# Optimization experiments

Measured on AMD Instinct MI355X. Metric: run time of the kernel, lower is better.

The kernel has to match this reference:

```python
import jax, jax.numpy as jnp
import numpy as np

D = 1024
H = 16
HD = D // H
FF = 4 * D
EPS = 1e-5


def _layernorm(x, scale, shift):
    # Faithful to the torch module: unbiased std (ddof=1), eps added to std.
    mean = jnp.mean(x, axis=-1, keepdims=True)
    var = jnp.sum((x - mean) ** 2, axis=-1, keepdims=True) / (x.shape[-1] - 1)
    std = jnp.sqrt(var)
    return shift + scale * (x - mean) / (std + EPS)


def _gelu(x):
    c = jnp.sqrt(jnp.asarray(2.0 / jnp.pi, dtype=x.dtype))
    return 0.5 * x * (1.0 + jnp.tanh(c * (x + 0.044715 * x ** 3)))


def setup_inputs() -> dict:
    key = jax.random.key(0)
    ks = jax.random.split(key, 8)
    B, S = 2, 2048
    inv = 1.0 / np.sqrt(D)
    x = jax.random.normal(ks[0], (B, S, D), dtype=jnp.float32)
    scale1 = jnp.ones((D,), jnp.float32)
    shift1 = jnp.zeros((D,), jnp.float32)
    Wqkv = jax.random.normal(ks[1], (3 * D, D), jnp.float32) * inv  # torch layout [out,in]
    Wo_w = jax.random.normal(ks[2], (D, D), jnp.float32) * inv
    Wo_b = jnp.zeros((D,), jnp.float32)
    scale2 = jnp.ones((D,), jnp.float32)
    shift2 = jnp.zeros((D,), jnp.float32)
    W1 = jax.random.normal(ks[3], (FF, D), jnp.float32) * inv
    b1 = jnp.zeros((FF,), jnp.float32)
    W2 = jax.random.normal(ks[4], (D, FF), jnp.float32) * (1.0 / np.sqrt(FF))
    b2 = jnp.zeros((D,), jnp.float32)
    return {"x": x, "scale1": scale1, "shift1": shift1, "Wqkv": Wqkv,
            "Wo_w": Wo_w, "Wo_b": Wo_b, "scale2": scale2, "shift2": shift2,
            "W1": W1, "b1": b1, "W2": W2, "b2": b2}


def reference(x, scale1, shift1, Wqkv, Wo_w, Wo_b, scale2, shift2, W1, b1, W2, b2):
    B, S, _ = x.shape
    # --- pre-norm attention ---
    h = _layernorm(x, scale1, shift1)
    qkv = jnp.einsum('bsd,ed->bse', h, Wqkv)  # [B,S,3D]
    q, k, v = jnp.split(qkv, 3, axis=-1)
    q = q.reshape(B, S, H, HD).transpose(0, 2, 1, 3)  # [B,H,S,HD]
    k = k.reshape(B, S, H, HD).transpose(0, 2, 1, 3)
    v = v.reshape(B, S, H, HD).transpose(0, 2, 1, 3)
    scores = jnp.einsum('bhqd,bhkd->bhqk', q, k) / jnp.sqrt(jnp.asarray(HD, x.dtype))
    causal = jnp.triu(jnp.ones((S, S), dtype=bool), k=1)
    scores = jnp.where(causal, -jnp.inf, scores)
    weights = jax.nn.softmax(scores, axis=-1)
    attn = jnp.einsum('bhqk,bhkd->bhqd', weights, v)
    attn = attn.transpose(0, 2, 1, 3).reshape(B, S, D)
    attn = jnp.einsum('bsd,ed->bse', attn, Wo_w) + Wo_b
    x = x + attn
    # --- pre-norm MLP ---
    h2 = _layernorm(x, scale2, shift2)
    m = _gelu(jnp.einsum('bsd,fd->bsf', h2, W1) + b1)
    m = jnp.einsum('bsf,df->bsd', m, W2) + b2
    return x + m
```

## Files before the change

kernel.cpp:

```cpp
#include <hip/hip_runtime.h>
#include <cstdint>
#include <cstddef>

typedef __bf16 bf16;
typedef __bf16 v8bf __attribute__((ext_vector_type(8)));
typedef __bf16 v4bf __attribute__((ext_vector_type(4)));
typedef float  v4f  __attribute__((ext_vector_type(4)));

#define D_MODEL 1024
#define FF_DIM  4096
#define SEQ     2048
#define NTOK    4096
#define NH      16
#define HDIM    64

#define GLOAD_LDS16(g, l) \
    __builtin_amdgcn_global_load_lds((const __attribute__((address_space(1))) void*)(g), \
                                     (__attribute__((address_space(3))) void*)(l), 16, 0, 0)

#define QSCALE 0.18033688011112042f
#define SHIFT2 -28.853900817779268f

#define BARRIER()    asm volatile("s_barrier" ::: "memory")
#define WAIT_VM8()   asm volatile("s_waitcnt vmcnt(8)" ::: "memory")
#define WAIT_VM0()   asm volatile("s_waitcnt vmcnt(0)" ::: "memory")
#define WAIT_LGKM0() asm volatile("s_waitcnt lgkmcnt(0)" ::: "memory")

__global__ __launch_bounds__(256) void prep_kernel(
    const float* __restrict__ Wqkv, const float* __restrict__ Wo,
    const float* __restrict__ W1, const float* __restrict__ W2,
    bf16* __restrict__ Wqkv_b, bf16* __restrict__ Wo_b,
    bf16* __restrict__ W1_b, bf16* __restrict__ W2_b) {
    int u = blockIdx.x * 256 + threadIdx.x;
    const float* src; bf16* dst; int idx;
    if (u < 786432)       { src = Wqkv; dst = Wqkv_b; idx = u * 4; }
    else if (u < 1048576) { src = Wo;   dst = Wo_b;   idx = (u - 786432) * 4; }
    else if (u < 2097152) { src = W1;   dst = W1_b;   idx = (u - 1048576) * 4; }
    else                  { src = W2;   dst = W2_b;   idx = (u - 2097152) * 4; }
    float4 v = *(const float4*)(src + idx);
    dst[idx + 0] = (bf16)v.x;
    dst[idx + 1] = (bf16)v.y;
    dst[idx + 2] = (bf16)v.z;
    dst[idx + 3] = (bf16)v.w;
}

__global__ __launch_bounds__(256) void layernorm_kernel(
    const float* __restrict__ x, const float* __restrict__ scale,
    const float* __restrict__ shift, bf16* __restrict__ out) {
    int row = blockIdx.x;
    int t = threadIdx.x;
    const float* xr = x + (size_t)row * D_MODEL;
    float4 v = *(const float4*)(xr + t * 4);
    float s  = v.x + v.y + v.z + v.w;
    float sq = v.x * v.x + v.y * v.y + v.z * v.z + v.w * v.w;
    #pragma unroll
    for (int o = 1; o < 64; o <<= 1) {
        s  += __shfl_xor(s, o);
        sq += __shfl_xor(sq, o);
    }
    __shared__ float ws[8];
    int wv = t >> 6;
    if ((t & 63) == 0) { ws[wv * 2] = s; ws[wv * 2 + 1] = sq; }
    __syncthreads();
    s  = ws[0] + ws[2] + ws[4] + ws[6];
    sq = ws[1] + ws[3] + ws[5] + ws[7];
    float mean = s * (1.0f / D_MODEL);
    float var  = (sq - (float)D_MODEL * mean * mean) * (1.0f / (D_MODEL - 1));
    var = fmaxf(var, 0.0f);
    float inv = 1.0f / (sqrtf(var) + 1e-5f);
    #pragma unroll
    for (int j = 0; j < 4; ++j) {
        int c = t * 4 + j;
        float xv = (&v.x)[j];
        out[(size_t)row * D_MODEL + c] = (bf16)(shift[c] + scale[c] * (xv - mean) * inv);
    }
}

__global__ __launch_bounds__(256) void transpose_v(
    const bf16* __restrict__ vb, bf16* __restrict__ vt) {
    int bh = blockIdx.x >> 5;
    int ts = blockIdx.x & 31;
    int t = threadIdx.x;
    __shared__ bf16 T[64][72];
    const bf16* src = vb + ((size_t)bh * SEQ + ts * 64) * HDIM;
    #pragma unroll
    for (int half = 0; half < 2; ++half) {
        int s = (t >> 3) + half * 32;
        int d0 = (t & 7) * 8;
        v8bf vv = *(const v8bf*)(src + (size_t)s * HDIM + d0);
        #pragma unroll
        for (int j = 0; j < 8; ++j) T[d0 + j][s] = vv[j];
    }
    __syncthreads();
    bf16* dst = vt + (size_t)bh * HDIM * SEQ + ts * 64;
    int d = t >> 2;
    #pragma unroll
    for (int cc = 0; cc < 2; ++cc) {
        int c = (t & 3) + cc * 4;
        v8bf o = *(const v8bf*)(&T[d][c * 8]);
        *(v8bf*)(dst + (size_t)d * SEQ + c * 8) = o;
    }
}

template <int EPI>
__global__ __launch_bounds__(256) void gemm_nt(
    const bf16* __restrict__ A, const bf16* __restrict__ Bw,
    const float* __restrict__ bias, const float* __restrict__ resid,
    float* __restrict__ outf, bf16* __restrict__ ob0,
    bf16* __restrict__ ob1, bf16* __restrict__ ob2,
    int M, int N, int K, int klen) {
    __shared__ __align__(16) bf16 As[128 * 64];
    __shared__ __align__(16) bf16 Bs[128 * 64];
    int gx = gridDim.x;
    int lin = blockIdx.y * gx + blockIdx.x;
    int grpsz = 16 * gx;
    int group = lin / grpsz;
    int rem = lin - group * grpsz;
    int m_t = group * 16 + (rem & 15);
    int n_t = rem >> 4;
    int m0 = m_t * 128, n0 = n_t * 128;
    int kstart = blockIdx.z * klen;
    int t = threadIdx.x;
    int lane = t & 63, wave = t >> 6;
    int wm = wave >> 1, wn = wave & 1;
    int quad = lane >> 4, l16 = lane & 15;

    int srow8 = lane >> 3;
    int schunk = (lane & 7) ^ srow8;
    const bf16* agp = A  + (size_t)(m0 + wave * 8 + srow8) * K + kstart + schunk * 8;
    const bf16* bgp = Bw + (size_t)(n0 + wave * 8 + srow8) * K + kstart + schunk * 8;
    size_t row32 = (size_t)32 * K;

    v4f acc[4][4];
    #pragma unroll
    for (int i = 0; i < 4; ++i)
        #pragma unroll
        for (int j = 0; j < 4; ++j)
            acc[i][j] = (v4f){0.f, 0.f, 0.f, 0.f};

    int rsw = l16 & 7;
    for (int kk = 0; kk < klen; kk += 64) {
        __syncthreads();
        #pragma unroll
        for (int ii = 0; ii < 4; ++ii) {
            GLOAD_LDS16(agp + ii * row32 + kk, &As[ii * 2048 + wave * 512]);
            GLOAD_LDS16(bgp + ii * row32 + kk, &Bs[ii * 2048 + wave * 512]);
        }
        __syncthreads();
        #pragma unroll
        for (int h = 0; h < 2; ++h) {
            v8bf af[4], bfr[4];
            #pragma unroll
            for (int i = 0; i < 4; ++i)
                af[i] = *(const v8bf*)(&As[(wm * 64 + i * 16 + l16) * 64 + (((h * 4 + quad) ^ rsw)) * 8]);
            #pragma unroll
            for (int j = 0; j < 4; ++j)
                bfr[j] = *(const v8bf*)(&Bs[(wn * 64 + j * 16 + l16) * 64 + (((h * 4 + quad) ^ rsw)) * 8]);
            #pragma unroll
            for (int i = 0; i < 4; ++i)
                #pragma unroll
                for (int j = 0; j < 4; ++j)
                    acc[i][j] = __builtin_amdgcn_mfma_f32_16x16x32_bf16(af[i], bfr[j], acc[i][j], 0, 0, 0);
        }
    }

    #pragma unroll
    for (int i = 0; i < 4; ++i) {
        #pragma unroll
        for (int j = 0; j < 4; ++j) {
            #pragma unroll
            for (int r = 0; r < 4; ++r) {
                float v = acc[i][j][r];
                int row = m0 + wm * 64 + i * 16 + quad * 4 + r;
                int col = n0 + wn * 64 + j * 16 + l16;
                if (EPI == 1) {
                    size_t o = (size_t)row * N + col;
                    outf[o] = resid[o] + v + bias[col];
                }
            }
        }
    }
}

template <int EPI>
__global__ __launch_bounds__(512, 2) void gemm2_nt(
    const bf16* __restrict__ A, const bf16* __restrict__ Bw,
    const float* __restrict__ bias, bf16* __restrict__ ob0,
    bf16* __restrict__ ob1, bf16* __restrict__ ob2,
    int M, int N, int K, int klen) {
    __shared__ __align__(16) bf16 smA[2][256 * 64];
    __shared__ __align__(16) bf16 smB[2][256 * 64];

    int m0 = blockIdx.y * 256, n0 = blockIdx.x * 256;
    int kstart = blockIdx.z * klen;
    int t = threadIdx.x;
    int lane = t & 63, wave = t >> 6;
    int wm = wave >> 2, wn = wave & 3;
    int quad = lane >> 4, l16 = lane & 15;

    int srow8 = lane >> 3;
    int schunk = (lane & 7) ^ srow8;
    const bf16* aA = A  + (size_t)(m0 + wave * 8 + srow8) * K + kstart + schunk * 8;
    const bf16* bB = Bw + (size_t)(n0 + wave * 8 + srow8) * K + kstart + schunk * 8;
    size_t row64 = (size_t)64 * K;
    int NT = klen >> 6;

    v4f acc[8][4];
    #pragma unroll
    for (int i = 0; i < 8; ++i)
        #pragma unroll
        for (int j = 0; j < 4; ++j)
            acc[i][j] = (v4f){0.f, 0.f, 0.f, 0.f};

    auto stage = [&](int c, int kt) {
        size_t ko = (size_t)kt * 64;
        const bf16* ag = aA + ko;
        const bf16* bg = bB + ko;
        #pragma unroll
        for (int q = 0; q < 4; ++q) {
            GLOAD_LDS16(ag + q * row64, &smA[c][q * 4096 + wave * 512]);
            GLOAD_LDS16(bg + q * row64, &smB[c][q * 4096 + wave * 512]);
        }
    };

    stage(0, 0);
    if (NT > 1) { stage(1, 1); WAIT_VM8(); } else { WAIT_VM0(); }
    BARRIER();

    int rx = l16 & 7;
    int ch0 = (quad ^ rx) * 8;
    int ch1 = ch0 ^ 32;
    int arow = (wm * 128 + l16) * 64;
    int brow = (wn * 64 + l16) * 64;

    for (int kt = 0; kt < NT; ++kt) {
        int c = kt & 1;
        const bf16* Ab = &smA[c][arow];
        const bf16* Bb = &smB[c][brow];
        v8bf a[4][2], b[4][2];
        #pragma unroll
        for (int i = 0; i < 4; ++i) {
            a[i][0] = *(const v8bf*)(Ab + i * 1024 + ch0);
            a[i][1] = *(const v8bf*)(Ab + i * 1024 + ch1);
        }
        #pragma unroll
        for (int j = 0; j < 4; ++j) {
            b[j][0] = *(const v8bf*)(Bb + j * 1024 + ch0);
            b[j][1] = *(const v8bf*)(Bb + j * 1024 + ch1);
        }
        __builtin_amdgcn_s_setprio(1);
        #pragma unroll
        for (int i = 0; i < 4; ++i)
            #pragma unroll
            for (int j = 0; j < 2; ++j) {
                acc[i][j] = __builtin_amdgcn_mfma_f32_16x16x32_bf16(a[i][0], b[j][0], acc[i][j], 0, 0, 0);
                acc[i][j] = __builtin_amdgcn_mfma_f32_16x16x32_bf16(a[i][1], b[j][1], acc[i][j], 0, 0, 0);
            }
        __builtin_amdgcn_s_setprio(0);
        __builtin_amdgcn_s_setprio(1);
        #pragma unroll
        for (int i = 0; i < 4; ++i)
            #pragma unroll
            for (int j = 2; j < 4; ++j) {
                acc[i][j] = __builtin_amdgcn_mfma_f32_16x16x32_bf16(a[i][0], b[j][0], acc[i][j], 0, 0, 0);
                acc[i][j] = __builtin_amdgcn_mfma_f32_16x16x32_bf16(a[i][1], b[j][1], acc[i][j], 0, 0, 0);
            }
        __builtin_amdgcn_s_setprio(0);
        #pragma unroll
        for (int i = 0; i < 4; ++i) {
            a[i][0] = *(const v8bf*)(Ab + 4096 + i * 1024 + ch0);
            a[i][1] = *(const v8bf*)(Ab + 4096 + i * 1024 + ch1);
        }
        __builtin_amdgcn_s_setprio(1);
        #pragma unroll
        for (int i = 0; i < 4; ++i)
            #pragma unroll
            for (int j = 0; j < 2; ++j) {
                acc[i + 4][j] = __builtin_amdgcn_mfma_f32_16x16x32_bf16(a[i][0], b[j][0], acc[i + 4][j], 0, 0, 0);
                acc[i + 4][j] = __builtin_amdgcn_mfma_f32_16x16x32_bf16(a[i][1], b[j][1], acc[i + 4][j], 0, 0, 0);
            }
        __builtin_amdgcn_s_setprio(0);
        WAIT_LGKM0();
        BARRIER();
        if (kt + 2 < NT) stage(c, kt + 2);
        __builtin_amdgcn_s_setprio(1);
        #pragma unroll
        for (int i = 0; i < 4; ++i)
            #pragma unroll
            for (int j = 2; j < 4; ++j) {
                acc[i + 4][j] = __builtin_amdgcn_mfma_f32_16x16x32_bf16(a[i][0], b[j][0], acc[i + 4][j], 0, 0, 0);
                acc[i + 4][j] = __builtin_amdgcn_mfma_f32_16x16x32_bf16(a[i][1], b[j][1], acc[i + 4][j], 0, 0, 0);
            }
        __builtin_amdgcn_s_setprio(0);
        if (kt + 1 < NT) {
            if (kt + 2 < NT) WAIT_VM8();
            else             WAIT_VM0();
            BARRIER();
        }
    }

    #pragma unroll
    for (int i = 0; i < 8; ++i) {
        #pragma unroll
        for (int j = 0; j < 4; ++j) {
            #pragma unroll
            for (int r = 0; r < 4; ++r) {
                float v = acc[i][j][r];
                int row = m0 + wm * 128 + i * 16 + quad * 4 + r;
                int col = n0 + wn * 64 + j * 16 + l16;
                if (EPI == 0) {
                    int which = col >> 10, rr = col & 1023;
                    int h = rr >> 6, d = rr & 63;
                    int bb = row >> 11, sI = row & 2047;
                    size_t dst = (((size_t)(bb * NH + h)) * SEQ + sI) * HDIM + d;
                    if (which == 0)      ob0[dst] = (bf16)(v * QSCALE);
                    else if (which == 1) ob1[dst] = (bf16)v;
                    else                 ob2[dst] = (bf16)v;
                } else if (EPI == 2) {
                    float u = v + bias[col];
                    float y = 1.5957691216057308f * (u + 0.044715f * u * u * u);
                    float g = u * __builtin_amdgcn_rcpf(1.0f + __expf(-y));
                    ob0[(size_t)row * N + col] = (bf16)g;
                } else {
                    ob0[(size_t)blockIdx.z * M * N + (size_t)row * N + col] = (bf16)v;
                }
            }
        }
    }
}

__global__ __launch_bounds__(256) void combine_w2(
    const bf16* __restrict__ part, const float* __restrict__ x1,
    const float* __restrict__ b2, float* __restrict__ out) {
    int i = (blockIdx.x * 256 + threadIdx.x) * 4;
    int col = i & (D_MODEL - 1);
    float4 xv = *(const float4*)(x1 + i);
    float4 bv = *(const float4*)(b2 + col);
    float4 r;
    r.x = xv.x + bv.x; r.y = xv.y + bv.y; r.z = xv.z + bv.z; r.w = xv.w + bv.w;
    #pragma unroll
    for (int z = 0; z < 4; ++z) {
        v4bf p = *(const v4bf*)(part + (size_t)z * NTOK * D_MODEL + i);
        r.x += (float)p[0]; r.y += (float)p[1]; r.z += (float)p[2]; r.w += (float)p[3];
    }
    *(float4*)(out + i) = r;
}

__device__ __forceinline__ void attn_process_tile(
    int kv, int qwb, int quad, int l16,
    const bf16* Ks, const bf16* Vs, bf16* Pw,
    const v8bf& qf0, const v8bf& qf1, v4f (&o)[4], float& lsum) {
    #pragma unroll
    for (int hh = 0; hh < 2; ++hh) {
        int kb32 = kv + hh * 32;
        if (kb32 > qwb + 15) break;
        #pragma unroll
        for (int j2 = 0; j2 < 2; ++j2) {
            int j = hh * 2 + j2;
            int kb16 = kb32 + j2 * 16;
            union { bf16 h[4]; uint2 u; } pk;
            if (kb16 > qwb + 15) {
                pk.u = (uint2){0u, 0u};
            } else {
                int key = j * 16 + l16;
                v8bf ka = *(const v8bf*)(&Ks[(key * 8 + (quad ^ (key & 7))) * 8]);
                v8bf kc = *(const v8bf*)(&Ks[(key * 8 + ((quad + 4) ^ (key & 7))) * 8]);
                v4f s = (v4f){SHIFT2, SHIFT2, SHIFT2, SHIFT2};
                s = __builtin_amdgcn_mfma_f32_16x16x32_bf16(ka, qf0, s, 0, 0, 0);
                s = __builtin_amdgcn_mfma_f32_16x16x32_bf16(kc, qf1, s, 0, 0, 0);
                bool dm = (kb16 + 15 > qwb);
                int keyb = kb16 + quad * 4;
                #pragma unroll
                for (int r = 0; r < 4; ++r) {
                    float pv = __builtin_amdgcn_exp2f(s[r]);
                    if (dm) pv = (keyb + r <= qwb + l16) ? pv : 0.f;
                    lsum += pv;
                    pk.h[r] = (bf16)pv;
                }
            }
            *(uint2*)(&Pw[l16 * 80 + j * 16 + quad * 4]) = pk.u;
        }
        v8bf pf = *(const v8bf*)(&Pw[l16 * 80 + hh * 32 + quad * 8]);
        #pragma unroll
        for (int dc = 0; dc < 4; ++dc) {
            int dim = dc * 16 + l16;
            v8bf vv = *(const v8bf*)(&Vs[(dim * 8 + ((quad + 4 * hh) ^ (dim & 7))) * 8]);
            o[dc] = __builtin_amdgcn_mfma_f32_16x16x32_bf16(pf, vv, o[dc], 0, 0, 0);
        }
    }
}

__global__ __launch_bounds__(256) void attn_kernel(
    const bf16* __restrict__ qb, const bf16* __restrict__ kb,
    const bf16* __restrict__ vt, bf16* __restrict__ ob) {
    int bh = blockIdx.x & 31;
    int pr = blockIdx.x >> 5;
    int qtA = pr, qtB = 31 - pr;

    int t = threadIdx.x;
    int wave = t >> 6, lane = t & 63;
    int quad = lane >> 4, l16 = lane & 15;
    int qwbA = qtA * 64 + wave * 16;
    int qwbB = qtB * 64 + wave * 16;

    const bf16* Qh  = qb + (size_t)bh * SEQ * HDIM;
    const bf16* Kh  = kb + (size_t)bh * SEQ * HDIM;
    const bf16* Vth = vt + (size_t)bh * HDIM * SEQ;

    __shared__ __align__(16) bf16 Ks[64 * 64];
    __shared__ __align__(16) bf16 Vs[64 * 64];
    __shared__ __align__(16) bf16 Ps[4][16 * 80];
    bf16* Pw = &Ps[wave][0];

    int u0 = t, u1 = t + 256;
    int key0 = u0 >> 3, c0 = (u0 & 7) ^ (key0 & 7);
    int key1 = u1 >> 3, c1 = (u1 & 7) ^ (key1 & 7);
    bf16* kdst0 = &Ks[wave * 512];
    bf16* kdst1 = &Ks[2048 + wave * 512];
    bf16* vdst0 = &Vs[wave * 512];
    bf16* vdst1 = &Vs[2048 + wave * 512];
    const bf16* Ksrc0 = Kh + (size_t)key0 * HDIM + c0 * 8;
    const bf16* Ksrc1 = Kh + (size_t)key1 * HDIM + c1 * 8;
    const bf16* Vsrc0 = Vth + (size_t)key0 * SEQ + c0 * 8;
    const bf16* Vsrc1 = Vth + (size_t)key1 * SEQ + c1 * 8;

    v8bf qfA0 = *(const v8bf*)(Qh + (size_t)(qwbA + l16) * HDIM + quad * 8);
    v8bf qfA1 = *(const v8bf*)(Qh + (size_t)(qwbA + l16) * HDIM + 32 + quad * 8);
    v8bf qfB0 = *(const v8bf*)(Qh + (size_t)(qwbB + l16) * HDIM + quad * 8);
    v8bf qfB1 = *(const v8bf*)(Qh + (size_t)(qwbB + l16) * HDIM + 32 + quad * 8);

    v4f oA[4], oB[4];
    #pragma unroll
    for (int dc = 0; dc < 4; ++dc) {
        oA[dc] = (v4f){0.f, 0.f, 0.f, 0.f};
        oB[dc] = (v4f){0.f, 0.f, 0.f, 0.f};
    }
    float lA = 0.f, lB = 0.f;

    int kvendA = qtA * 64 + 64;
    int kvendB = qtB * 64 + 64;
    for (int kv = 0; kv < kvendB; kv += 64) {
        __syncthreads();
        GLOAD_LDS16(Ksrc0 + (size_t)kv * HDIM, kdst0);
        GLOAD_LDS16(Ksrc1 + (size_t)kv * HDIM, kdst1);
        GLOAD_LDS16(Vsrc0 + kv, vdst0);
        GLOAD_LDS16(Vsrc1 + kv, vdst1);
        __syncthreads();
        if (kv < kvendA)
            attn_process_tile(kv, qwbA, quad, l16, Ks, Vs, Pw, qfA0, qfA1, oA, lA);
        attn_process_tile(kv, qwbB, quad, l16, Ks, Vs, Pw, qfB0, qfB1, oB, lB);
    }

    lA += __shfl_xor(lA, 16); lA += __shfl_xor(lA, 32);
    lB += __shfl_xor(lB, 16); lB += __shfl_xor(lB, 32);

    int b = bh >> 4, h = bh & 15;
    #pragma unroll
    for (int r = 0; r < 4; ++r) {
        float invA = 1.0f / __shfl(lA, quad * 4 + r);
        float invB = 1.0f / __shfl(lB, quad * 4 + r);
        int sA = qwbA + quad * 4 + r;
        int sB = qwbB + quad * 4 + r;
        #pragma unroll
        for (int dc = 0; dc < 4; ++dc) {
            int d = dc * 16 + l16;
            ob[((size_t)(b * SEQ + sA)) * D_MODEL + h * HDIM + d] = (bf16)(oA[dc][r] * invA);
            ob[((size_t)(b * SEQ + sB)) * D_MODEL + h * HDIM + d] = (bf16)(oB[dc][r] * invB);
        }
    }
}

extern "C" void kernel_launch(void* const* d_in, const int* in_sizes, int n_in,
                              void* d_out, int out_size, void* d_ws, size_t ws_size,
                              hipStream_t stream) {
    const float* x      = (const float*)d_in[0];
    const float* scale1 = (const float*)d_in[1];
    const float* shift1 = (const float*)d_in[2];
    const float* Wqkv   = (const float*)d_in[3];
    const float* Wo_w   = (const float*)d_in[4];
    const float* Wo_b   = (const float*)d_in[5];
    const float* scale2 = (const float*)d_in[6];
    const float* shift2 = (const float*)d_in[7];
    const float* W1     = (const float*)d_in[8];
    const float* b1     = (const float*)d_in[9];
    const float* W2     = (const float*)d_in[10];
    const float* b2     = (const float*)d_in[11];
    float* out = (float*)d_out;

    char* ws = (char*)d_ws;
    size_t off = 0;
    auto alloc = [&](size_t bytes) -> char* {
        char* p = ws + off;
        off += (bytes + 255) & ~(size_t)255;
        return p;
    };
    bf16* Wqkv_b = (bf16*)alloc((size_t)3 * D_MODEL * D_MODEL * 2);
    bf16* Wo_bf  = (bf16*)alloc((size_t)D_MODEL * D_MODEL * 2);
    bf16* W1_b   = (bf16*)alloc((size_t)FF_DIM * D_MODEL * 2);
    bf16* W2_b   = (bf16*)alloc((size_t)D_MODEL * FF_DIM * 2);
    bf16* bufA   = (bf16*)alloc((size_t)NTOK * D_MODEL * 2);
    bf16* qb     = (bf16*)alloc((size_t)NTOK * D_MODEL * 2);
    bf16* kb     = (bf16*)alloc((size_t)NTOK * D_MODEL * 2);
    bf16* vb     = (bf16*)alloc((size_t)NTOK * D_MODEL * 2);
    bf16* vtb    = (bf16*)alloc((size_t)NTOK * D_MODEL * 2);
    float* x1    = (float*)alloc((size_t)NTOK * D_MODEL * 4);
    bf16* mbuf   = (bf16*)alloc((size_t)NTOK * FF_DIM * 2);
    bf16* w2part = bufA;
    (void)ws_size; (void)n_in; (void)in_sizes; (void)out_size;

    prep_kernel<<<12288, 256, 0, stream>>>(Wqkv, Wo_w, W1, W2,
                                           Wqkv_b, Wo_bf, W1_b, W2_b);

    layernorm_kernel<<<NTOK, 256, 0, stream>>>(x, scale1, shift1, bufA);

    gemm2_nt<0><<<dim3(3072 / 256, NTOK / 256), 512, 0, stream>>>(
        bufA, Wqkv_b, nullptr, qb, kb, vb, NTOK, 3072, D_MODEL, D_MODEL);

    transpose_v<<<1024, 256, 0, stream>>>(vb, vtb);

    attn_kernel<<<512, 256, 0, stream>>>(qb, kb, vtb, bufA);

    gemm_nt<1><<<dim3(D_MODEL / 128, NTOK / 128), 256, 0, stream>>>(
        bufA, Wo_bf, Wo_b, x, x1, nullptr, nullptr, nullptr, NTOK, D_MODEL, D_MODEL, D_MODEL);

    layernorm_kernel<<<NTOK, 256, 0, stream>>>(x1, scale2, shift2, qb);

    gemm2_nt<2><<<dim3(FF_DIM / 256, NTOK / 256), 512, 0, stream>>>(
        qb, W1_b, b1, mbuf, nullptr, nullptr, NTOK, FF_DIM, D_MODEL, D_MODEL);

    gemm2_nt<6><<<dim3(D_MODEL / 256, NTOK / 256, 4), 512, 0, stream>>>(
        mbuf, W2_b, nullptr, w2part, nullptr, nullptr, NTOK, D_MODEL, FF_DIM, FF_DIM / 4);

    combine_w2<<<NTOK * D_MODEL / 1024, 256, 0, stream>>>(w2part, x1, b2, out);
}
```

Baseline: 323.8 us.

## Double-buffer attention K/V tiles and fuse paired query-tile processing

The attention kernel now keeps two LDS buffers for K/V tiles and prefetches the tile two steps ahead with global-to-LDS loads, using vmcnt waits so the next tile's load overlaps the current tile's compute. The two query tiles (A and B) are processed together per key-tile, sharing the K and V fragment reads from LDS and interleaving their MFMAs. The P scratch buffers are split per query tile and XOR-swizzled to reduce LDS bank conflicts. In exchange it doubles LDS use and adds register pressure, which may lower occupancy.

```diff
diff --git a/kernel.cpp b/kernel.cpp
--- a/kernel.cpp
+++ b/kernel.cpp
@@ -23,6 +23,7 @@
 
 #define BARRIER()    asm volatile("s_barrier" ::: "memory")
 #define WAIT_VM8()   asm volatile("s_waitcnt vmcnt(8)" ::: "memory")
+#define WAIT_VM4()   asm volatile("s_waitcnt vmcnt(4)" ::: "memory")
 #define WAIT_VM0()   asm volatile("s_waitcnt vmcnt(0)" ::: "memory")
 #define WAIT_LGKM0() asm volatile("s_waitcnt lgkmcnt(0)" ::: "memory")
 
@@ -346,46 +347,82 @@
     *(float4*)(out + i) = r;
 }
 
-__device__ __forceinline__ void attn_process_tile(
-    int kv, int qwb, int quad, int l16,
-    const bf16* Ks, const bf16* Vs, bf16* Pw,
-    const v8bf& qf0, const v8bf& qf1, v4f (&o)[4], float& lsum) {
+__device__ __forceinline__ void attn_tile_pair(
+    int kv, int qwbA, int qwbB, bool doA, int quad, int l16, int sw,
+    const bf16* Ks, const bf16* Vs, bf16* PwA, bf16* PwB,
+    const v8bf& qfA0, const v8bf& qfA1, const v8bf& qfB0, const v8bf& qfB1,
+    v4f (&oA)[4], v4f (&oB)[4], float& lA, float& lB) {
     #pragma unroll
     for (int hh = 0; hh < 2; ++hh) {
         int kb32 = kv + hh * 32;
-        if (kb32 > qwb + 15) break;
+        if (kb32 > qwbB + 15) break;
+        bool aH = doA && (kb32 <= qwbA + 15);
         #pragma unroll
         for (int j2 = 0; j2 < 2; ++j2) {
             int j = hh * 2 + j2;
             int kb16 = kb32 + j2 * 16;
-            union { bf16 h[4]; uint2 u; } pk;
-            if (kb16 > qwb + 15) {
-                pk.u = (uint2){0u, 0u};
-            } else {
-                int key = j * 16 + l16;
-                v8bf ka = *(const v8bf*)(&Ks[(key * 8 + (quad ^ (key & 7))) * 8]);
-                v8bf kc = *(const v8bf*)(&Ks[(key * 8 + ((quad + 4) ^ (key & 7))) * 8]);
-                v4f s = (v4f){SHIFT2, SHIFT2, SHIFT2, SHIFT2};
-                s = __builtin_amdgcn_mfma_f32_16x16x32_bf16(ka, qf0, s, 0, 0, 0);
-                s = __builtin_amdgcn_mfma_f32_16x16x32_bf16(kc, qf1, s, 0, 0, 0);
-                bool dm = (kb16 + 15 > qwb);
-                int keyb = kb16 + quad * 4;
-                #pragma unroll
-                for (int r = 0; r < 4; ++r) {
-                    float pv = __builtin_amdgcn_exp2f(s[r]);
-                    if (dm) pv = (keyb + r <= qwb + l16) ? pv : 0.f;
-                    lsum += pv;
-                    pk.h[r] = (bf16)pv;
+            int key = j * 16 + l16;
+            v8bf ka = *(const v8bf*)(&Ks[(key * 8 + (quad ^ (key & 7))) * 8]);
+            v8bf kc = *(const v8bf*)(&Ks[(key * 8 + ((quad + 4) ^ (key & 7))) * 8]);
+            int poff = l16 * 80 + ((j * 4 + quad) ^ sw) * 4;
+            int keyb = kb16 + quad * 4;
+            {
+                union { bf16 h[4]; uint2 u; } pk;
+                if (kb16 > qwbB + 15) {
+                    pk.u = (uint2){0u, 0u};
+                } else {
+                    v4f s = (v4f){SHIFT2, SHIFT2, SHIFT2, SHIFT2};
+                    s = __builtin_amdgcn_mfma_f32_16x16x32_bf16(ka, qfB0, s, 0, 0, 0);
+                    s = __builtin_amdgcn_mfma_f32_16x16x32_bf16(kc, qfB1, s, 0, 0, 0);
+                    bool dm = (kb16 + 15 > qwbB);
+                    #pragma unroll
+                    for (int r = 0; r < 4; ++r) {
+                        float pv = __builtin_amdgcn_exp2f(s[r]);
+                        if (dm) pv = (keyb + r <= qwbB + l16) ? pv : 0.f;
+                        lB += pv;
+                        pk.h[r] = (bf16)pv;
+                    }
                 }
-            }
-            *(uint2*)(&Pw[l16 * 80 + j * 16 + quad * 4]) = pk.u;
-        }
-        v8bf pf = *(const v8bf*)(&Pw[l16 * 80 + hh * 32 + quad * 8]);
-        #pragma unroll
-        for (int dc = 0; dc < 4; ++dc) {
-            int dim = dc * 16 + l16;
-            v8bf vv = *(const v8bf*)(&Vs[(dim * 8 + ((quad + 4 * hh) ^ (dim & 7))) * 8]);
-            o[dc] = __builtin_amdgcn_mfma_f32_16x16x32_bf16(pf, vv, o[dc], 0, 0, 0);
+                *(uint2*)(&PwB[poff]) = pk.u;
+            }
+            if (aH) {
+                union { bf16 h[4]; uint2 u; } pk;
+                if (kb16 > qwbA + 15) {
+                    pk.u = (uint2){0u, 0u};
+                } else {
+                    v4f s = (v4f){SHIFT2, SHIFT2, SHIFT2, SHIFT2};
+                    s = __builtin_amdgcn_mfma_f32_16x16x32_bf16(ka, qfA0, s, 0, 0, 0);
+                    s = __builtin_amdgcn_mfma_f32_16x16x32_bf16(kc, qfA1, s, 0, 0, 0);
+                    bool dm = (kb16 + 15 > qwbA);
+                    #pragma unroll
+                    for (int r = 0; r < 4; ++r) {
+                        float pv = __builtin_amdgcn_exp2f(s[r]);
+                        if (dm) pv = (keyb + r <= qwbA + l16) ? pv : 0.f;
+                        lA += pv;
+                        pk.h[r] = (bf16)pv;
+                    }
+                }
+                *(uint2*)(&PwA[poff]) = pk.u;
+            }
+        }
+        int roff = l16 * 80 + (((hh * 4 + quad) * 2) ^ sw) * 4;
+        v8bf pfB = *(const v8bf*)(&PwB[roff]);
+        if (aH) {
+            v8bf pfA = *(const v8bf*)(&PwA[roff]);
+            #pragma unroll
+            for (int dc = 0; dc < 4; ++dc) {
+                int dim = dc * 16 + l16;
+                v8bf vv = *(const v8bf*)(&Vs[(dim * 8 + ((quad + 4 * hh) ^ (dim & 7))) * 8]);
+                oB[dc] = __builtin_amdgcn_mfma_f32_16x16x32_bf16(pfB, vv, oB[dc], 0, 0, 0);
+                oA[dc] = __builtin_amdgcn_mfma_f32_16x16x32_bf16(pfA, vv, oA[dc], 0, 0, 0);
+            }
+        } else {
+            #pragma unroll
+            for (int dc = 0; dc < 4; ++dc) {
+                int dim = dc * 16 + l16;
+                v8bf vv = *(const v8bf*)(&Vs[(dim * 8 + ((quad + 4 * hh) ^ (dim & 7))) * 8]);
+                oB[dc] = __builtin_amdgcn_mfma_f32_16x16x32_bf16(pfB, vv, oB[dc], 0, 0, 0);
+            }
         }
     }
 }
@@ -400,6 +437,7 @@
     int t = threadIdx.x;
     int wave = t >> 6, lane = t & 63;
     int quad = lane >> 4, l16 = lane & 15;
+    int sw = l16 & 12;
     int qwbA = qtA * 64 + wave * 16;
     int qwbB = qtB * 64 + wave * 16;
 
@@ -407,23 +445,27 @@
     const bf16* Kh  = kb + (size_t)bh * SEQ * HDIM;
     const bf16* Vth = vt + (size_t)bh * HDIM * SEQ;
 
-    __shared__ __align__(16) bf16 Ks[64 * 64];
-    __shared__ __align__(16) bf16 Vs[64 * 64];
-    __shared__ __align__(16) bf16 Ps[4][16 * 80];
-    bf16* Pw = &Ps[wave][0];
+    __shared__ __align__(16) bf16 Ks[2][64 * 64];
+    __shared__ __align__(16) bf16 Vs[2][64 * 64];
+    __shared__ __align__(16) bf16 Ps[4][2][16 * 80];
+    bf16* PwA = &Ps[wave][0][0];
+    bf16* PwB = &Ps[wave][1][0];
 
     int u0 = t, u1 = t + 256;
     int key0 = u0 >> 3, c0 = (u0 & 7) ^ (key0 & 7);
     int key1 = u1 >> 3, c1 = (u1 & 7) ^ (key1 & 7);
-    bf16* kdst0 = &Ks[wave * 512];
-    bf16* kdst1 = &Ks[2048 + wave * 512];
-    bf16* vdst0 = &Vs[wave * 512];
-    bf16* vdst1 = &Vs[2048 + wave * 512];
     const bf16* Ksrc0 = Kh + (size_t)key0 * HDIM + c0 * 8;
     const bf16* Ksrc1 = Kh + (size_t)key1 * HDIM + c1 * 8;
     const bf16* Vsrc0 = Vth + (size_t)key0 * SEQ + c0 * 8;
     const bf16* Vsrc1 = Vth + (size_t)key1 * SEQ + c1 * 8;
 
+    auto stage = [&](int c, int kv) {
+        GLOAD_LDS16(Ksrc0 + (size_t)kv * HDIM, &Ks[c][wave * 512]);
+        GLOAD_LDS16(Ksrc1 + (size_t)kv * HDIM, &Ks[c][2048 + wave * 512]);
+        GLOAD_LDS16(Vsrc0 + kv, &Vs[c][wave * 512]);
+        GLOAD_LDS16(Vsrc1 + kv, &Vs[c][2048 + wave * 512]);
+    };
+
     v8bf qfA0 = *(const v8bf*)(Qh + (size_t)(qwbA + l16) * HDIM + quad * 8);
     v8bf qfA1 = *(const v8bf*)(Qh + (size_t)(qwbA + l16) * HDIM + 32 + quad * 8);
     v8bf qfB0 = *(const v8bf*)(Qh + (size_t)(qwbB + l16) * HDIM + quad * 8);
@@ -437,18 +479,27 @@
     }
     float lA = 0.f, lB = 0.f;
 
-    int kvendA = qtA * 64 + 64;
-    int kvendB = qtB * 64 + 64;
-    for (int kv = 0; kv < kvendB; kv += 64) {
-        __syncthreads();
-        GLOAD_LDS16(Ksrc0 + (size_t)kv * HDIM, kdst0);
-        GLOAD_LDS16(Ksrc1 + (size_t)kv * HDIM, kdst1);
-        GLOAD_LDS16(Vsrc0 + kv, vdst0);
-        GLOAD_LDS16(Vsrc1 + kv, vdst1);
-        __syncthreads();
-        if (kv < kvendA)
-            attn_process_tile(kv, qwbA, quad, l16, Ks, Vs, Pw, qfA0, qfA1, oA, lA);
-        attn_process_tile(kv, qwbB, quad, l16, Ks, Vs, Pw, qfB0, qfB1, oB, lB);
+    int nt = qtB + 1;
+    stage(0, 0);
+    stage(1, 64);
+    WAIT_VM4();
+    BARRIER();
+
+    for (int ti = 0; ti < nt; ++ti) {
+        int c = ti & 1;
+        int kv = ti * 64;
+        bool doA = (ti <= qtA);
+        attn_tile_pair(kv, qwbA, qwbB, doA, quad, l16, sw,
+                       &Ks[c][0], &Vs[c][0], PwA, PwB,
+                       qfA0, qfA1, qfB0, qfB1, oA, oB, lA, lB);
+        WAIT_LGKM0();
+        BARRIER();
+        if (ti + 2 < nt) stage(c, kv + 128);
+        if (ti + 1 < nt) {
+            if (ti + 2 < nt) WAIT_VM4();
+            else             WAIT_VM0();
+            BARRIER();
+        }
     }
 
     lA += __shfl_xor(lA, 16); lA += __shfl_xor(lA, 32);
```

Result: slower. 331.2 us (+2.3%).

## Split attention KV tiles across two wave groups and compute row sums via MFMA

Applied to the files above, without the earlier changes.

The attention kernel now runs 512 threads as two groups of four waves. Each group handles alternate 64-key tiles, loaded together into a doubled K/V shared buffer, and the partial outputs are reduced through shared memory at the end. The per-element softmax row-sum accumulation is replaced by an extra MFMA of P against a ones vector, which removes scalar adds and cross-lane shuffles. This raises parallelism per block and trades more LDS use and a final reduction for fewer serial KV iterations.

```diff
diff --git a/kernel.cpp b/kernel.cpp
--- a/kernel.cpp
+++ b/kernel.cpp
@@ -348,8 +348,8 @@
 
 __device__ __forceinline__ void attn_process_tile(
     int kv, int qwb, int quad, int l16,
-    const bf16* Ks, const bf16* Vs, bf16* Pw,
-    const v8bf& qf0, const v8bf& qf1, v4f (&o)[4], float& lsum) {
+    const bf16* Ks, const bf16* Vs, bf16* Pw, const v8bf& ones,
+    const v8bf& qf0, const v8bf& qf1, v4f (&o)[4], v4f& o5) {
     #pragma unroll
     for (int hh = 0; hh < 2; ++hh) {
         int kb32 = kv + hh * 32;
@@ -374,13 +374,13 @@
                 for (int r = 0; r < 4; ++r) {
                     float pv = __builtin_amdgcn_exp2f(s[r]);
                     if (dm) pv = (keyb + r <= qwb + l16) ? pv : 0.f;
-                    lsum += pv;
                     pk.h[r] = (bf16)pv;
                 }
             }
             *(uint2*)(&Pw[l16 * 80 + j * 16 + quad * 4]) = pk.u;
         }
         v8bf pf = *(const v8bf*)(&Pw[l16 * 80 + hh * 32 + quad * 8]);
+        o5 = __builtin_amdgcn_mfma_f32_16x16x32_bf16(pf, ones, o5, 0, 0, 0);
         #pragma unroll
         for (int dc = 0; dc < 4; ++dc) {
             int dim = dc * 16 + l16;
@@ -390,7 +390,7 @@
     }
 }
 
-__global__ __launch_bounds__(256) void attn_kernel(
+__global__ __launch_bounds__(512, 4) void attn_kernel(
     const bf16* __restrict__ qb, const bf16* __restrict__ kb,
     const bf16* __restrict__ vt, bf16* __restrict__ ob) {
     int bh = blockIdx.x & 31;
@@ -399,73 +399,117 @@
 
     int t = threadIdx.x;
     int wave = t >> 6, lane = t & 63;
+    int g = wave >> 2, wv = wave & 3;
     int quad = lane >> 4, l16 = lane & 15;
-    int qwbA = qtA * 64 + wave * 16;
-    int qwbB = qtB * 64 + wave * 16;
+    int qwbA = qtA * 64 + wv * 16;
+    int qwbB = qtB * 64 + wv * 16;
 
     const bf16* Qh  = qb + (size_t)bh * SEQ * HDIM;
     const bf16* Kh  = kb + (size_t)bh * SEQ * HDIM;
     const bf16* Vth = vt + (size_t)bh * HDIM * SEQ;
 
-    __shared__ __align__(16) bf16 Ks[64 * 64];
-    __shared__ __align__(16) bf16 Vs[64 * 64];
-    __shared__ __align__(16) bf16 Ps[4][16 * 80];
-    bf16* Pw = &Ps[wave][0];
-
-    int u0 = t, u1 = t + 256;
-    int key0 = u0 >> 3, c0 = (u0 & 7) ^ (key0 & 7);
-    int key1 = u1 >> 3, c1 = (u1 & 7) ^ (key1 & 7);
-    bf16* kdst0 = &Ks[wave * 512];
-    bf16* kdst1 = &Ks[2048 + wave * 512];
-    bf16* vdst0 = &Vs[wave * 512];
-    bf16* vdst1 = &Vs[2048 + wave * 512];
-    const bf16* Ksrc0 = Kh + (size_t)key0 * HDIM + c0 * 8;
-    const bf16* Ksrc1 = Kh + (size_t)key1 * HDIM + c1 * 8;
-    const bf16* Vsrc0 = Vth + (size_t)key0 * SEQ + c0 * 8;
-    const bf16* Vsrc1 = Vth + (size_t)key1 * SEQ + c1 * 8;
+    __shared__ __align__(16) char smem_raw[53248];
+    bf16* Ks  = (bf16*)smem_raw;
+    bf16* Vs  = (bf16*)(smem_raw + 16384);
+    bf16* Pw  = (bf16*)(smem_raw + 32768) + wave * 1280;
+    float* scr = (float*)smem_raw;
+
+    int key = t >> 3;
+    int cch = (t & 7) ^ (key & 7);
+    const bf16* Ksrc = Kh + (size_t)key * HDIM + cch * 8;
+    const bf16* Vsrc = Vth + (size_t)key * SEQ + cch * 8;
+    bf16* kdst0 = Ks + wave * 512;
+    bf16* kdst1 = Ks + 4096 + wave * 512;
+    bf16* vdst0 = Vs + wave * 512;
+    bf16* vdst1 = Vs + 4096 + wave * 512;
 
     v8bf qfA0 = *(const v8bf*)(Qh + (size_t)(qwbA + l16) * HDIM + quad * 8);
     v8bf qfA1 = *(const v8bf*)(Qh + (size_t)(qwbA + l16) * HDIM + 32 + quad * 8);
     v8bf qfB0 = *(const v8bf*)(Qh + (size_t)(qwbB + l16) * HDIM + quad * 8);
     v8bf qfB1 = *(const v8bf*)(Qh + (size_t)(qwbB + l16) * HDIM + 32 + quad * 8);
 
+    v8bf ones;
+    #pragma unroll
+    for (int j = 0; j < 8; ++j) ones[j] = (bf16)1.0f;
+
     v4f oA[4], oB[4];
     #pragma unroll
     for (int dc = 0; dc < 4; ++dc) {
         oA[dc] = (v4f){0.f, 0.f, 0.f, 0.f};
         oB[dc] = (v4f){0.f, 0.f, 0.f, 0.f};
     }
-    float lA = 0.f, lB = 0.f;
-
-    int kvendA = qtA * 64 + 64;
-    int kvendB = qtB * 64 + 64;
-    for (int kv = 0; kv < kvendB; kv += 64) {
+    v4f o5A = (v4f){0.f, 0.f, 0.f, 0.f};
+    v4f o5B = (v4f){0.f, 0.f, 0.f, 0.f};
+
+    int nt = qtB + 1;
+    int nit = (nt + 1) >> 1;
+    for (int it = 0; it < nit; ++it) {
+        int t0 = 2 * it;
+        int t1 = t0 + 1;
         __syncthreads();
-        GLOAD_LDS16(Ksrc0 + (size_t)kv * HDIM, kdst0);
-        GLOAD_LDS16(Ksrc1 + (size_t)kv * HDIM, kdst1);
-        GLOAD_LDS16(Vsrc0 + kv, vdst0);
-        GLOAD_LDS16(Vsrc1 + kv, vdst1);
+        GLOAD_LDS16(Ksrc + (size_t)(t0 * 64) * HDIM, kdst0);
+        GLOAD_LDS16(Vsrc + t0 * 64, vdst0);
+        if (t1 < nt) {
+            GLOAD_LDS16(Ksrc + (size_t)(t1 * 64) * HDIM, kdst1);
+            GLOAD_LDS16(Vsrc + t1 * 64, vdst1);
+        }
         __syncthreads();
-        if (kv < kvendA)
-            attn_process_tile(kv, qwbA, quad, l16, Ks, Vs, Pw, qfA0, qfA1, oA, lA);
-        attn_process_tile(kv, qwbB, quad, l16, Ks, Vs, Pw, qfB0, qfB1, oB, lB);
-    }
-
-    lA += __shfl_xor(lA, 16); lA += __shfl_xor(lA, 32);
-    lB += __shfl_xor(lB, 16); lB += __shfl_xor(lB, 32);
-
-    int b = bh >> 4, h = bh & 15;
-    #pragma unroll
-    for (int r = 0; r < 4; ++r) {
-        float invA = 1.0f / __shfl(lA, quad * 4 + r);
-        float invB = 1.0f / __shfl(lB, quad * 4 + r);
-        int sA = qwbA + quad * 4 + r;
-        int sB = qwbB + quad * 4 + r;
-        #pragma unroll
-        for (int dc = 0; dc < 4; ++dc) {
-            int d = dc * 16 + l16;
-            ob[((size_t)(b * SEQ + sA)) * D_MODEL + h * HDIM + d] = (bf16)(oA[dc][r] * invA);
-            ob[((size_t)(b * SEQ + sB)) * D_MODEL + h * HDIM + d] = (bf16)(oB[dc][r] * invB);
+        int ti = t0 + g;
+        if (ti < nt) {
+            int kv = ti * 64;
+            const bf16* Kst = Ks + g * 4096;
+            const bf16* Vst = Vs + g * 4096;
+            if (ti <= qtA)
+                attn_process_tile(kv, qwbA, quad, l16, Kst, Vst, Pw, ones,
+                                  qfA0, qfA1, oA, o5A);
+            attn_process_tile(kv, qwbB, quad, l16, Kst, Vst, Pw, ones,
+                              qfB0, qfB1, oB, o5B);
+        }
+    }
+
+    __syncthreads();
+    int sbase = wv * 2560 + lane;
+    if (g == 1) {
+        #pragma unroll
+        for (int dc = 0; dc < 4; ++dc)
+            #pragma unroll
+            for (int r = 0; r < 4; ++r) {
+                scr[sbase + (dc * 4 + r) * 64]        = oA[dc][r];
+                scr[sbase + (16 + dc * 4 + r) * 64]   = oB[dc][r];
+            }
+        #pragma unroll
+        for (int r = 0; r < 4; ++r) {
+            scr[sbase + (32 + r) * 64] = o5A[r];
+            scr[sbase + (36 + r) * 64] = o5B[r];
+        }
+    }
+    __syncthreads();
+    if (g == 0) {
+        #pragma unroll
+        for (int dc = 0; dc < 4; ++dc)
+            #pragma unroll
+            for (int r = 0; r < 4; ++r) {
+                oA[dc][r] += scr[sbase + (dc * 4 + r) * 64];
+                oB[dc][r] += scr[sbase + (16 + dc * 4 + r) * 64];
+            }
+        #pragma unroll
+        for (int r = 0; r < 4; ++r) {
+            o5A[r] += scr[sbase + (32 + r) * 64];
+            o5B[r] += scr[sbase + (36 + r) * 64];
+        }
+        int b = bh >> 4, h = bh & 15;
+        #pragma unroll
+        for (int r = 0; r < 4; ++r) {
+            float invA = 1.0f / o5A[r];
+            float invB = 1.0f / o5B[r];
+            int sA = qwbA + quad * 4 + r;
+            int sB = qwbB + quad * 4 + r;
+            #pragma unroll
+            for (int dc = 0; dc < 4; ++dc) {
+                int d = dc * 16 + l16;
+                ob[((size_t)(b * SEQ + sA)) * D_MODEL + h * HDIM + d] = (bf16)(oA[dc][r] * invA);
+                ob[((size_t)(b * SEQ + sB)) * D_MODEL + h * HDIM + d] = (bf16)(oB[dc][r] * invB);
+            }
         }
     }
 }
@@ -518,7 +562,7 @@
 
     transpose_v<<<1024, 256, 0, stream>>>(vb, vtb);
 
-    attn_kernel<<<512, 256, 0, stream>>>(qb, kb, vtb, bufA);
+    attn_kernel<<<512, 512, 0, stream>>>(qb, kb, vtb, bufA);
 
     gemm_nt<1><<<dim3(D_MODEL / 128, NTOK / 128), 256, 0, stream>>>(
         bufA, Wo_bf, Wo_b, x, x1, nullptr, nullptr, nullptr, NTOK, D_MODEL, D_MODEL, D_MODEL);
```

Measured after the change: 313.4 us. -3.2%, faster.

## Double-buffer attention KV tiles, one q-tile per block, MFMA row sums, swizzle GEMM grid

Applied to the files above, without the earlier changes.

The attention kernel changes from pairing two query tiles per block to one query tile per block, launching 1024 blocks in heaviest-first order. K/V tiles are now double-buffered in LDS with global_load_lds prefetch and vmcnt waits, so loads overlap compute. The softmax denominator is computed with an MFMA against a ones vector instead of scalar adds and shuffles, and the P row stride shrinks to 72. The bf16 GEMM also remaps workgroup IDs with an XCD-style swizzle to improve L2 locality. The trade-offs are more LDS per block and a possible loss of load balance from the unpaired tiles.

```diff
diff --git a/kernel.cpp b/kernel.cpp
--- a/kernel.cpp
+++ b/kernel.cpp
@@ -23,6 +23,7 @@
 
 #define BARRIER()    asm volatile("s_barrier" ::: "memory")
 #define WAIT_VM8()   asm volatile("s_waitcnt vmcnt(8)" ::: "memory")
+#define WAIT_VM4()   asm volatile("s_waitcnt vmcnt(4)" ::: "memory")
 #define WAIT_VM0()   asm volatile("s_waitcnt vmcnt(0)" ::: "memory")
 #define WAIT_LGKM0() asm volatile("s_waitcnt lgkmcnt(0)" ::: "memory")
 
@@ -191,7 +192,14 @@
     __shared__ __align__(16) bf16 smA[2][256 * 64];
     __shared__ __align__(16) bf16 smB[2][256 * 64];
 
-    int m0 = blockIdx.y * 256, n0 = blockIdx.x * 256;
+    int gx = gridDim.x, gy = gridDim.y;
+    int nwg = gx * gy;
+    int lin = blockIdx.y * gx + blockIdx.x;
+    int q8 = nwg >> 3;
+    int swz = (lin & 7) * q8 + (lin >> 3);
+    int m_t = swz % gy;
+    int n_t = swz / gy;
+    int m0 = m_t * 256, n0 = n_t * 256;
     int kstart = blockIdx.z * klen;
     int t = threadIdx.x;
     int lane = t & 63, wave = t >> 6;
@@ -348,8 +356,8 @@
 
 __device__ __forceinline__ void attn_process_tile(
     int kv, int qwb, int quad, int l16,
-    const bf16* Ks, const bf16* Vs, bf16* Pw,
-    const v8bf& qf0, const v8bf& qf1, v4f (&o)[4], float& lsum) {
+    const bf16* Ks, const bf16* Vs, bf16* Pw, const v8bf& ones,
+    const v8bf& qf0, const v8bf& qf1, v4f (&o)[4], v4f& o5) {
     #pragma unroll
     for (int hh = 0; hh < 2; ++hh) {
         int kb32 = kv + hh * 32;
@@ -374,13 +382,13 @@
                 for (int r = 0; r < 4; ++r) {
                     float pv = __builtin_amdgcn_exp2f(s[r]);
                     if (dm) pv = (keyb + r <= qwb + l16) ? pv : 0.f;
-                    lsum += pv;
                     pk.h[r] = (bf16)pv;
                 }
             }
-            *(uint2*)(&Pw[l16 * 80 + j * 16 + quad * 4]) = pk.u;
-        }
-        v8bf pf = *(const v8bf*)(&Pw[l16 * 80 + hh * 32 + quad * 8]);
+            *(uint2*)(&Pw[l16 * 72 + j * 16 + quad * 4]) = pk.u;
+        }
+        v8bf pf = *(const v8bf*)(&Pw[l16 * 72 + hh * 32 + quad * 8]);
+        o5 = __builtin_amdgcn_mfma_f32_16x16x32_bf16(pf, ones, o5, 0, 0, 0);
         #pragma unroll
         for (int dc = 0; dc < 4; ++dc) {
             int dim = dc * 16 + l16;
@@ -390,82 +398,75 @@
     }
 }
 
-__global__ __launch_bounds__(256) void attn_kernel(
+__global__ __launch_bounds__(256, 4) void attn_kernel(
     const bf16* __restrict__ qb, const bf16* __restrict__ kb,
     const bf16* __restrict__ vt, bf16* __restrict__ ob) {
     int bh = blockIdx.x & 31;
-    int pr = blockIdx.x >> 5;
-    int qtA = pr, qtB = 31 - pr;
+    int qt = 31 - (blockIdx.x >> 5);
 
     int t = threadIdx.x;
     int wave = t >> 6, lane = t & 63;
     int quad = lane >> 4, l16 = lane & 15;
-    int qwbA = qtA * 64 + wave * 16;
-    int qwbB = qtB * 64 + wave * 16;
+    int qwb = qt * 64 + wave * 16;
 
     const bf16* Qh  = qb + (size_t)bh * SEQ * HDIM;
     const bf16* Kh  = kb + (size_t)bh * SEQ * HDIM;
     const bf16* Vth = vt + (size_t)bh * HDIM * SEQ;
 
-    __shared__ __align__(16) bf16 Ks[64 * 64];
-    __shared__ __align__(16) bf16 Vs[64 * 64];
-    __shared__ __align__(16) bf16 Ps[4][16 * 80];
-    bf16* Pw = &Ps[wave][0];
-
-    int u0 = t, u1 = t + 256;
-    int key0 = u0 >> 3, c0 = (u0 & 7) ^ (key0 & 7);
-    int key1 = u1 >> 3, c1 = (u1 & 7) ^ (key1 & 7);
-    bf16* kdst0 = &Ks[wave * 512];
-    bf16* kdst1 = &Ks[2048 + wave * 512];
-    bf16* vdst0 = &Vs[wave * 512];
-    bf16* vdst1 = &Vs[2048 + wave * 512];
-    const bf16* Ksrc0 = Kh + (size_t)key0 * HDIM + c0 * 8;
-    const bf16* Ksrc1 = Kh + (size_t)key1 * HDIM + c1 * 8;
-    const bf16* Vsrc0 = Vth + (size_t)key0 * SEQ + c0 * 8;
-    const bf16* Vsrc1 = Vth + (size_t)key1 * SEQ + c1 * 8;
-
-    v8bf qfA0 = *(const v8bf*)(Qh + (size_t)(qwbA + l16) * HDIM + quad * 8);
-    v8bf qfA1 = *(const v8bf*)(Qh + (size_t)(qwbA + l16) * HDIM + 32 + quad * 8);
-    v8bf qfB0 = *(const v8bf*)(Qh + (size_t)(qwbB + l16) * HDIM + quad * 8);
-    v8bf qfB1 = *(const v8bf*)(Qh + (size_t)(qwbB + l16) * HDIM + 32 + quad * 8);
-
-    v4f oA[4], oB[4];
-    #pragma unroll
-    for (int dc = 0; dc < 4; ++dc) {
-        oA[dc] = (v4f){0.f, 0.f, 0.f, 0.f};
-        oB[dc] = (v4f){0.f, 0.f, 0.f, 0.f};
-    }
-    float lA = 0.f, lB = 0.f;
-
-    int kvendA = qtA * 64 + 64;
-    int kvendB = qtB * 64 + 64;
-    for (int kv = 0; kv < kvendB; kv += 64) {
-        __syncthreads();
-        GLOAD_LDS16(Ksrc0 + (size_t)kv * HDIM, kdst0);
-        GLOAD_LDS16(Ksrc1 + (size_t)kv * HDIM, kdst1);
-        GLOAD_LDS16(Vsrc0 + kv, vdst0);
-        GLOAD_LDS16(Vsrc1 + kv, vdst1);
-        __syncthreads();
-        if (kv < kvendA)
-            attn_process_tile(kv, qwbA, quad, l16, Ks, Vs, Pw, qfA0, qfA1, oA, lA);
-        attn_process_tile(kv, qwbB, quad, l16, Ks, Vs, Pw, qfB0, qfB1, oB, lB);
-    }
-
-    lA += __shfl_xor(lA, 16); lA += __shfl_xor(lA, 32);
-    lB += __shfl_xor(lB, 16); lB += __shfl_xor(lB, 32);
+    __shared__ __align__(16) bf16 Ks[2][4096];
+    __shared__ __align__(16) bf16 Vs[2][4096];
+    __shared__ __align__(16) bf16 Ps[4][1152];
+    bf16* Pw = Ps[wave];
+
+    int key = t >> 3;
+    int cch = (t & 7) ^ (key & 7);
+    const bf16* Ksrc = Kh + (size_t)key * HDIM + cch * 8;
+    const bf16* Vsrc = Vth + (size_t)key * SEQ + cch * 8;
+
+    v8bf qf0 = *(const v8bf*)(Qh + (size_t)(qwb + l16) * HDIM + quad * 8);
+    v8bf qf1 = *(const v8bf*)(Qh + (size_t)(qwb + l16) * HDIM + 32 + quad * 8);
+
+    auto stage = [&](int c, int kv) {
+        GLOAD_LDS16(Ksrc + (size_t)kv * HDIM,        &Ks[c][wave * 512]);
+        GLOAD_LDS16(Ksrc + (size_t)(kv + 32) * HDIM, &Ks[c][2048 + wave * 512]);
+        GLOAD_LDS16(Vsrc + kv,                        &Vs[c][wave * 512]);
+        GLOAD_LDS16(Vsrc + (size_t)32 * SEQ + kv,     &Vs[c][2048 + wave * 512]);
+    };
+
+    v8bf ones;
+    #pragma unroll
+    for (int j = 0; j < 8; ++j) ones[j] = (bf16)1.0f;
+
+    v4f o[4];
+    #pragma unroll
+    for (int dc = 0; dc < 4; ++dc) o[dc] = (v4f){0.f, 0.f, 0.f, 0.f};
+    v4f o5 = (v4f){0.f, 0.f, 0.f, 0.f};
+
+    int nt = qt + 1;
+    stage(0, 0);
+    for (int ti = 0; ti < nt; ++ti) {
+        int c = ti & 1;
+        if (ti + 1 < nt) {
+            stage(c ^ 1, (ti + 1) * 64);
+            WAIT_VM4();
+        } else {
+            WAIT_VM0();
+        }
+        BARRIER();
+        attn_process_tile(ti * 64, qwb, quad, l16, Ks[c], Vs[c], Pw, ones,
+                          qf0, qf1, o, o5);
+        BARRIER();
+    }
 
     int b = bh >> 4, h = bh & 15;
     #pragma unroll
     for (int r = 0; r < 4; ++r) {
-        float invA = 1.0f / __shfl(lA, quad * 4 + r);
-        float invB = 1.0f / __shfl(lB, quad * 4 + r);
-        int sA = qwbA + quad * 4 + r;
-        int sB = qwbB + quad * 4 + r;
+        float inv = 1.0f / o5[r];
+        int s = qwb + quad * 4 + r;
         #pragma unroll
         for (int dc = 0; dc < 4; ++dc) {
             int d = dc * 16 + l16;
-            ob[((size_t)(b * SEQ + sA)) * D_MODEL + h * HDIM + d] = (bf16)(oA[dc][r] * invA);
-            ob[((size_t)(b * SEQ + sB)) * D_MODEL + h * HDIM + d] = (bf16)(oB[dc][r] * invB);
+            ob[((size_t)(b * SEQ + s)) * D_MODEL + h * HDIM + d] = (bf16)(o[dc][r] * inv);
         }
     }
 }
@@ -518,7 +519,7 @@
 
     transpose_v<<<1024, 256, 0, stream>>>(vb, vtb);
 
-    attn_kernel<<<512, 256, 0, stream>>>(qb, kb, vtb, bufA);
+    attn_kernel<<<1024, 256, 0, stream>>>(qb, kb, vtb, bufA);
 
     gemm_nt<1><<<dim3(D_MODEL / 128, NTOK / 128), 256, 0, stream>>>(
         bufA, Wo_bf, Wo_b, x, x1, nullptr, nullptr, nullptr, NTOK, D_MODEL, D_MODEL, D_MODEL);
```

Measured after the change: 320.7 us. Within noise of the previous version (-0.9%).
